# Kernel optimization log

Hardware: AMD Instinct MI355X
Metric: run time of the kernel (lower is better)

## Reference

```python
import jax, jax.numpy as jnp
import numpy as np
import math

QUERY_DIM = 128
SCALE = 1.0 / math.sqrt(QUERY_DIM)

def setup_inputs() -> dict:
    key = jax.random.key(0)
    k1, k2, k3 = jax.random.split(key, 3)
    B, Q, K, D = 16, 2048, 2048, 128
    return {
        "query": jax.random.normal(k1, (B, Q, D), dtype=jnp.float32),
        "keys": jax.random.normal(k2, (B, K, D), dtype=jnp.float32),
        "values": jax.random.normal(k3, (B, K, D), dtype=jnp.float32),
    }

def reference(query, keys, values):
    # energy[b,q,k] = sum_d query[b,q,d] * keys[b,k,d], scaled then softmax over k
    energy = jnp.einsum("bqd,bkd->bqk", query, keys) * SCALE
    attn = jax.nn.softmax(energy, axis=2)
    # linear combination over values
    return jnp.einsum("bqk,bkv->bqv", attn, values)
```

## Files before the change

kernel.cpp:

```cpp
#include <hip/hip_runtime.h>
#include <hip/hip_bf16.h>


#define BATCH 16
#define QLEN 2048
#define KLEN 2048
#define DIM 128
#define BM 64
#define BN 64
#define NT (KLEN / BN)

#define SMEM_BYTES 34048

typedef __attribute__((ext_vector_type(8))) short bf16x8;
typedef __attribute__((ext_vector_type(4))) float f32x4;

__device__ __forceinline__ short f2bf(float x) {
    union { float f; unsigned u; } v; v.f = x;
    unsigned r = v.u + 0x7FFFu + ((v.u >> 16) & 1u);
    return (short)(r >> 16);
}
__device__ __forceinline__ unsigned pkbf(float a, float b) {
    union { float f; unsigned u; } x, y; x.f = a; y.f = b;
    unsigned ra = x.u + 0x7FFFu + ((x.u >> 16) & 1u);
    unsigned rb = y.u + 0x7FFFu + ((y.u >> 16) & 1u);
    return __builtin_amdgcn_perm(rb, ra, 0x07060302u);
}
__device__ __forceinline__ float fexp2(float x) {
#if __has_builtin(__builtin_amdgcn_exp2f)
    return __builtin_amdgcn_exp2f(x);
#else
    return exp2f(x);
#endif
}

#define TSTR 72
__global__ __launch_bounds__(256) void prepass_kernel(
    const float* __restrict__ kg, const float* __restrict__ vg,
    unsigned short* __restrict__ Kws, unsigned short* __restrict__ Vtws)
{
    __shared__ unsigned short T[DIM * TSTR];
    const int tid = threadIdx.x;
    const int kb  = blockIdx.x * BN;
    const int b   = blockIdx.y;
    const float* kt = kg + ((size_t)b * KLEN + kb) * DIM;
    const float* vt = vg + ((size_t)b * KLEN + kb) * DIM;

    unsigned short* koF = Kws + ((size_t)b * KLEN + kb) * DIM;
#pragma unroll
    for (int j = 0; j < 4; ++j) {
        int c = tid + 256 * j;
        int key   = c & 63;
        int chunk = c >> 6;
        float4 k0 = *(const float4*)(kt + key * DIM + chunk * 8);
        float4 k1 = *(const float4*)(kt + key * DIM + chunk * 8 + 4);
        uint4 w;
        w.x = pkbf(k0.x, k0.y); w.y = pkbf(k0.z, k0.w);
        w.z = pkbf(k1.x, k1.y); w.w = pkbf(k1.z, k1.w);
        int r    = (key & 3) | ((key & 8) >> 1) | ((key & 16) >> 1)
                 | ((key & 4) << 2) | (key & 32);
        int kw_  = r >> 5;
        int half = (r >> 4) & 1;
        int lm_  = r & 15;
        int dk   = chunk >> 2;
        int qd   = chunk & 3;
        int soff = (((kw_ * 4 + dk) * 2 + half) * 4 + qd) * 128 + lm_ * 8;
        *(uint4*)(koF + soff) = w;
    }

#pragma unroll
    for (int j = 0; j < 8; ++j) {
        int idx = tid + 256 * j;
        int key = idx >> 5;
        int d4  = (idx & 31) * 4;
        float4 vv = *(const float4*)(vt + key * DIM + d4);
        T[(d4 + 0) * TSTR + key] = (unsigned short)f2bf(vv.x);
        T[(d4 + 1) * TSTR + key] = (unsigned short)f2bf(vv.y);
        T[(d4 + 2) * TSTR + key] = (unsigned short)f2bf(vv.z);
        T[(d4 + 3) * TSTR + key] = (unsigned short)f2bf(vv.w);
    }
    __syncthreads();
    unsigned short* voF = Vtws + ((size_t)b * KLEN + kb) * DIM;
#pragma unroll
    for (int j = 0; j < 4; ++j) {
        int c = tid + 256 * j;
        int d = c >> 3;
        int g = c & 7;
        uint4 u = *(const uint4*)&T[d * TSTR + g * 8];
        int kw_  = g >> 2;
        int qd   = g & 3;
        int dt   = d >> 4;
        int lm_  = d & 15;
        int soff = ((kw_ * 8 + dt) * 4 + qd) * 128 + lm_ * 8;
        *(uint4*)(voF + soff) = u;
    }
}

__global__ __launch_bounds__(256, 2) void attn_flash_kernel(
    const float* __restrict__ qg,
    const unsigned short* __restrict__ Kws,
    const unsigned short* __restrict__ Vtws,
    float* __restrict__ outg)
{
    __shared__ __align__(16) char SMC[SMEM_BYTES];

    const int tid  = threadIdx.x;
    const int wave = tid >> 6;
    const int lane = tid & 63;
    const int lm   = lane & 15;
    const int quad = lane >> 4;
    const int rw   = wave >> 1;
    const int kw   = wave & 1;

    const int n  = blockIdx.y * gridDim.x + blockIdx.x;
    const int np = (n & 7) * 64 + (n >> 3);
    const int b     = np >> 5;
    const int qbase = (np & 31) * BM + rw * 32;

    const float QSCALE = 0.08838834764831845f * 1.4426950408889634f;

    bf16x8 qfA[4], qfB[4];
    {
        const float* qrowA = qg + (size_t)(b * QLEN + qbase + lm) * DIM;
        const float* qrowB = qrowA + 16 * DIM;
#pragma unroll
        for (int dk = 0; dk < 4; ++dk) {
            int d0 = dk * 32 + quad * 8;
            float4 a = *(const float4*)(qrowA + d0);
            float4 c = *(const float4*)(qrowA + d0 + 4);
            uint4 u;
            u.x = pkbf(a.x*QSCALE, a.y*QSCALE); u.y = pkbf(a.z*QSCALE, a.w*QSCALE);
            u.z = pkbf(c.x*QSCALE, c.y*QSCALE); u.w = pkbf(c.z*QSCALE, c.w*QSCALE);
            qfA[dk] = *(bf16x8*)&u;
            float4 e = *(const float4*)(qrowB + d0);
            float4 g = *(const float4*)(qrowB + d0 + 4);
            uint4 v;
            v.x = pkbf(e.x*QSCALE, e.y*QSCALE); v.y = pkbf(e.z*QSCALE, e.w*QSCALE);
            v.z = pkbf(g.x*QSCALE, g.y*QSCALE); v.w = pkbf(g.z*QSCALE, g.w*QSCALE);
            qfB[dk] = *(bf16x8*)&v;
        }
    }

    f32x4 OA[8], OB[8];
#pragma unroll
    for (int i = 0; i < 8; ++i) { OA[i] = 0.0f; OB[i] = 0.0f; }
    float lrA = 0.f, lrB = 0.f;

    const unsigned short* kfp = Kws + (size_t)b * KLEN * DIM
                              + kw * 4096 + lane * 8;
    const unsigned short* vfp = Vtws + (size_t)b * KLEN * DIM
                              + kw * 4096 + lane * 8;

    f32x4 SP0a, SP1a, SP0b, SP1b;
    bf16x8 vp[8];
    bf16x8 kp[8];

#pragma unroll
    for (int i = 0; i < 8; ++i) kp[i] = *(const bf16x8*)(kfp + i * 512);
#pragma unroll
    for (int i = 0; i < 8; ++i) vp[i] = *(const bf16x8*)(vfp + i * 512);
    {
        f32x4 S0a = 0.0f, S1a = 0.0f, S0b = 0.0f, S1b = 0.0f;
#pragma unroll
        for (int dk = 0; dk < 4; ++dk) {
            S0a = __builtin_amdgcn_mfma_f32_16x16x32_bf16(kp[2*dk],   qfA[dk], S0a, 0, 0, 0);
            S0b = __builtin_amdgcn_mfma_f32_16x16x32_bf16(kp[2*dk],   qfB[dk], S0b, 0, 0, 0);
            S1a = __builtin_amdgcn_mfma_f32_16x16x32_bf16(kp[2*dk+1], qfA[dk], S1a, 0, 0, 0);
            S1b = __builtin_amdgcn_mfma_f32_16x16x32_bf16(kp[2*dk+1], qfB[dk], S1b, 0, 0, 0);
        }
#pragma unroll
        for (int i = 0; i < 8; ++i)
            kp[i] = *(const bf16x8*)(kfp + 8192 + i * 512);
        SP0a = S0a; SP1a = S1a; SP0b = S0b; SP1b = S1b;
    }

    for (int t = 1; t < NT; ++t) {
        float a0 = fexp2(SP0a[0]), a1 = fexp2(SP0a[1]), a2 = fexp2(SP0a[2]), a3 = fexp2(SP0a[3]);
        float a4 = fexp2(SP1a[0]), a5 = fexp2(SP1a[1]), a6 = fexp2(SP1a[2]), a7 = fexp2(SP1a[3]);
        float b0 = fexp2(SP0b[0]), b1 = fexp2(SP0b[1]), b2 = fexp2(SP0b[2]), b3 = fexp2(SP0b[3]);
        float b4 = fexp2(SP1b[0]), b5 = fexp2(SP1b[1]), b6 = fexp2(SP1b[2]), b7 = fexp2(SP1b[3]);
        uint4 puA, puB;
        puA.x = pkbf(a0,a1); puA.y = pkbf(a2,a3); puA.z = pkbf(a4,a5); puA.w = pkbf(a6,a7);
        puB.x = pkbf(b0,b1); puB.y = pkbf(b2,b3); puB.z = pkbf(b4,b5); puB.w = pkbf(b6,b7);
        bf16x8 pfA = *(bf16x8*)&puA;
        bf16x8 pfB = *(bf16x8*)&puB;
        lrA += ((a0+a1)+(a2+a3)) + ((a4+a5)+(a6+a7));
        lrB += ((b0+b1)+(b2+b3)) + ((b4+b5)+(b6+b7));

        f32x4 S0a = 0.0f, S1a = 0.0f, S0b = 0.0f, S1b = 0.0f;
#pragma unroll
        for (int dk = 0; dk < 4; ++dk) {
            S0a = __builtin_amdgcn_mfma_f32_16x16x32_bf16(kp[2*dk],   qfA[dk], S0a, 0, 0, 0);
            S0b = __builtin_amdgcn_mfma_f32_16x16x32_bf16(kp[2*dk],   qfB[dk], S0b, 0, 0, 0);
            S1a = __builtin_amdgcn_mfma_f32_16x16x32_bf16(kp[2*dk+1], qfA[dk], S1a, 0, 0, 0);
            S1b = __builtin_amdgcn_mfma_f32_16x16x32_bf16(kp[2*dk+1], qfB[dk], S1b, 0, 0, 0);
        }

        if (t + 1 < NT) {
            const unsigned short* kt1 = kfp + (size_t)(t + 1) * 8192;
#pragma unroll
            for (int i = 0; i < 8; ++i)
                kp[i] = *(const bf16x8*)(kt1 + i * 512);
        }

#pragma unroll
        for (int dt = 0; dt < 8; ++dt) {
            OA[dt] = __builtin_amdgcn_mfma_f32_16x16x32_bf16(vp[dt], pfA, OA[dt], 0, 0, 0);
            OB[dt] = __builtin_amdgcn_mfma_f32_16x16x32_bf16(vp[dt], pfB, OB[dt], 0, 0, 0);
        }

        {
            const unsigned short* vt1 = vfp + (size_t)t * 8192;
#pragma unroll
            for (int dt = 0; dt < 8; ++dt)
                vp[dt] = *(const bf16x8*)(vt1 + dt * 512);
        }

        SP0a = S0a; SP1a = S1a; SP0b = S0b; SP1b = S1b;
    }

    {
        float a0 = fexp2(SP0a[0]), a1 = fexp2(SP0a[1]), a2 = fexp2(SP0a[2]), a3 = fexp2(SP0a[3]);
        float a4 = fexp2(SP1a[0]), a5 = fexp2(SP1a[1]), a6 = fexp2(SP1a[2]), a7 = fexp2(SP1a[3]);
        float b0 = fexp2(SP0b[0]), b1 = fexp2(SP0b[1]), b2 = fexp2(SP0b[2]), b3 = fexp2(SP0b[3]);
        float b4 = fexp2(SP1b[0]), b5 = fexp2(SP1b[1]), b6 = fexp2(SP1b[2]), b7 = fexp2(SP1b[3]);
        uint4 puA, puB;
        puA.x = pkbf(a0,a1); puA.y = pkbf(a2,a3); puA.z = pkbf(a4,a5); puA.w = pkbf(a6,a7);
        puB.x = pkbf(b0,b1); puB.y = pkbf(b2,b3); puB.z = pkbf(b4,b5); puB.w = pkbf(b6,b7);
        bf16x8 pfA = *(bf16x8*)&puA;
        bf16x8 pfB = *(bf16x8*)&puB;
        lrA += ((a0+a1)+(a2+a3)) + ((a4+a5)+(a6+a7));
        lrB += ((b0+b1)+(b2+b3)) + ((b4+b5)+(b6+b7));
#pragma unroll
        for (int dt = 0; dt < 8; ++dt) {
            OA[dt] = __builtin_amdgcn_mfma_f32_16x16x32_bf16(vp[dt], pfA, OA[dt], 0, 0, 0);
            OB[dt] = __builtin_amdgcn_mfma_f32_16x16x32_bf16(vp[dt], pfB, OB[dt], 0, 0, 0);
        }
    }

    lrA += __shfl_xor(lrA, 16, 64); lrA += __shfl_xor(lrA, 32, 64);
    lrB += __shfl_xor(lrB, 16, 64); lrB += __shfl_xor(lrB, 32, 64);

    float* Orw = (float*)SMC + rw * 4288;
    if (kw == 1) {
#pragma unroll
        for (int dt = 0; dt < 8; ++dt) {
            *(f32x4*)&Orw[lm*132        + dt*16 + quad*4] = OA[dt];
            *(f32x4*)&Orw[(16+lm)*132   + dt*16 + quad*4] = OB[dt];
        }
        if (lane < 16)      Orw[4224 + lm]      = lrA;
        else if (lane < 32) Orw[4224 + 16 + lm] = lrB;
    }
    __syncthreads();
    if (kw == 0) {
        float invA = 1.0f / (lrA + Orw[4224 + lm]);
        float invB = 1.0f / (lrB + Orw[4224 + 16 + lm]);
        float* orowA = outg + (size_t)(b * QLEN + qbase + lm) * DIM;
        float* orowB = orowA + 16 * DIM;
#pragma unroll
        for (int dt = 0; dt < 8; ++dt) {
            f32x4 oA = *(const f32x4*)&Orw[lm*132      + dt*16 + quad*4];
            f32x4 oB = *(const f32x4*)&Orw[(16+lm)*132 + dt*16 + quad*4];
            *(f32x4*)&orowA[dt*16 + quad*4] = (OA[dt] + oA) * invA;
            *(f32x4*)&orowB[dt*16 + quad*4] = (OB[dt] + oB) * invB;
        }
    }
}

extern "C" void kernel_launch(void* const* d_in, const int* in_sizes, int n_in,
                              void* d_out, int out_size, void* d_ws, size_t ws_size,
                              hipStream_t stream) {
    const float* q = (const float*)d_in[0];
    const float* k = (const float*)d_in[1];
    const float* v = (const float*)d_in[2];
    float* o = (float*)d_out;
    unsigned short* Kws  = (unsigned short*)d_ws;
    unsigned short* Vtws = Kws + (size_t)BATCH * KLEN * DIM;
    dim3 grid(KLEN / BN, BATCH);
    prepass_kernel<<<grid, 256, 0, stream>>>(k, v, Kws, Vtws);
    dim3 grid2(QLEN / BM, BATCH);
    attn_flash_kernel<<<grid2, 256, 0, stream>>>(q, Kws, Vtws, o);
}
```

Before: 136.5 us.

## Split keys across four waves per row group with 512-thread blocks

```diff
diff --git a/kernel.cpp b/kernel.cpp
--- a/kernel.cpp
+++ b/kernel.cpp
@@ -7,10 +7,11 @@
 #define KLEN 2048
 #define DIM 128
 #define BM 64
-#define BN 64
-#define NT (KLEN / BN)
-
-#define SMEM_BYTES 34048
+#define BNW 128
+#define NT (KLEN / BNW)
+#define TILE_SHORTS 8192
+
+#define SMEM_BYTES 34304
 
 typedef __attribute__((ext_vector_type(8))) short bf16x8;
 typedef __attribute__((ext_vector_type(4))) float f32x4;
@@ -37,11 +38,11 @@
 #define TSTR 72
 __global__ __launch_bounds__(256) void prepass_kernel(
     const float* __restrict__ kg, const float* __restrict__ vg,
-    unsigned short* __restrict__ Kws, unsigned short* __restrict__ Vtws)
+    unsigned short* __restrict__ Kws, unsigned short* __restrict__ Vws)
 {
     __shared__ unsigned short T[DIM * TSTR];
     const int tid = threadIdx.x;
-    const int kb  = blockIdx.x * BN;
+    const int kb  = blockIdx.x * 64;
     const int b   = blockIdx.y;
     const float* kt = kg + ((size_t)b * KLEN + kb) * DIM;
     const float* vt = vg + ((size_t)b * KLEN + kb) * DIM;
@@ -59,12 +60,12 @@
         w.z = pkbf(k1.x, k1.y); w.w = pkbf(k1.z, k1.w);
         int r    = (key & 3) | ((key & 8) >> 1) | ((key & 16) >> 1)
                  | ((key & 4) << 2) | (key & 32);
-        int kw_  = r >> 5;
+        int kh   = r >> 5;
         int half = (r >> 4) & 1;
         int lm_  = r & 15;
         int dk   = chunk >> 2;
         int qd   = chunk & 3;
-        int soff = (((kw_ * 4 + dk) * 2 + half) * 4 + qd) * 128 + lm_ * 8;
+        int soff = (((kh * 4 + dk) * 2 + half) * 4 + qd) * 128 + lm_ * 8;
         *(uint4*)(koF + soff) = w;
     }
 
@@ -80,26 +81,26 @@
         T[(d4 + 3) * TSTR + key] = (unsigned short)f2bf(vv.w);
     }
     __syncthreads();
-    unsigned short* voF = Vtws + ((size_t)b * KLEN + kb) * DIM;
+    unsigned short* voF = Vws + ((size_t)b * KLEN + kb) * DIM;
 #pragma unroll
     for (int j = 0; j < 4; ++j) {
         int c = tid + 256 * j;
         int d = c >> 3;
         int g = c & 7;
         uint4 u = *(const uint4*)&T[d * TSTR + g * 8];
-        int kw_  = g >> 2;
+        int kh   = g >> 2;
         int qd   = g & 3;
         int dt   = d >> 4;
         int lm_  = d & 15;
-        int soff = ((kw_ * 8 + dt) * 4 + qd) * 128 + lm_ * 8;
+        int soff = ((kh * 8 + dt) * 4 + qd) * 128 + lm_ * 8;
         *(uint4*)(voF + soff) = u;
     }
 }
 
-__global__ __launch_bounds__(256, 2) void attn_flash_kernel(
+__global__ __launch_bounds__(512, 4) void attn_flash_kernel(
     const float* __restrict__ qg,
     const unsigned short* __restrict__ Kws,
-    const unsigned short* __restrict__ Vtws,
+    const unsigned short* __restrict__ Vws,
     float* __restrict__ outg)
 {
     __shared__ __align__(16) char SMC[SMEM_BYTES];
@@ -109,8 +110,8 @@
     const int lane = tid & 63;
     const int lm   = lane & 15;
     const int quad = lane >> 4;
-    const int rw   = wave >> 1;
-    const int kw   = wave & 1;
+    const int rw   = wave >> 2;
+    const int kw   = wave & 3;
 
     const int n  = blockIdx.y * gridDim.x + blockIdx.x;
     const int np = (n & 7) * 64 + (n >> 3);
@@ -146,10 +147,9 @@
     for (int i = 0; i < 8; ++i) { OA[i] = 0.0f; OB[i] = 0.0f; }
     float lrA = 0.f, lrB = 0.f;
 
-    const unsigned short* kfp = Kws + (size_t)b * KLEN * DIM
-                              + kw * 4096 + lane * 8;
-    const unsigned short* vfp = Vtws + (size_t)b * KLEN * DIM
-                              + kw * 4096 + lane * 8;
+    const size_t woff = (size_t)(kw >> 1) * TILE_SHORTS + (kw & 1) * 4096 + lane * 8;
+    const unsigned short* kfp = Kws + (size_t)b * KLEN * DIM + woff;
+    const unsigned short* vfp = Vws + (size_t)b * KLEN * DIM + woff;
 
     f32x4 SP0a, SP1a, SP0b, SP1b;
     bf16x8 vp[8];
@@ -170,7 +170,7 @@
         }
 #pragma unroll
         for (int i = 0; i < 8; ++i)
-            kp[i] = *(const bf16x8*)(kfp + 8192 + i * 512);
+            kp[i] = *(const bf16x8*)(kfp + 2 * TILE_SHORTS + i * 512);
         SP0a = S0a; SP1a = S1a; SP0b = S0b; SP1b = S1b;
     }
 
@@ -197,7 +197,7 @@
         }
 
         if (t + 1 < NT) {
-            const unsigned short* kt1 = kfp + (size_t)(t + 1) * 8192;
+            const unsigned short* kt1 = kfp + (size_t)(t + 1) * (2 * TILE_SHORTS);
 #pragma unroll
             for (int i = 0; i < 8; ++i)
                 kp[i] = *(const bf16x8*)(kt1 + i * 512);
@@ -210,7 +210,7 @@
         }
 
         {
-            const unsigned short* vt1 = vfp + (size_t)t * 8192;
+            const unsigned short* vt1 = vfp + (size_t)t * (2 * TILE_SHORTS);
 #pragma unroll
             for (int dt = 0; dt < 8; ++dt)
                 vp[dt] = *(const bf16x8*)(vt1 + dt * 512);
@@ -242,27 +242,38 @@
     lrB += __shfl_xor(lrB, 16, 64); lrB += __shfl_xor(lrB, 32, 64);
 
     float* Orw = (float*)SMC + rw * 4288;
-    if (kw == 1) {
-#pragma unroll
-        for (int dt = 0; dt < 8; ++dt) {
-            *(f32x4*)&Orw[lm*132        + dt*16 + quad*4] = OA[dt];
-            *(f32x4*)&Orw[(16+lm)*132   + dt*16 + quad*4] = OB[dt];
-        }
-        if (lane < 16)      Orw[4224 + lm]      = lrA;
-        else if (lane < 32) Orw[4224 + 16 + lm] = lrB;
-    }
-    __syncthreads();
+#pragma unroll
+    for (int s = 3; s >= 1; --s) {
+        if (kw == s) {
+#pragma unroll
+            for (int dt = 0; dt < 8; ++dt) {
+                *(f32x4*)&Orw[lm*132        + dt*16 + quad*4] = OA[dt];
+                *(f32x4*)&Orw[(16+lm)*132   + dt*16 + quad*4] = OB[dt];
+            }
+            if (lane < 16)      Orw[4224 + lm]      = lrA;
+            else if (lane < 32) Orw[4224 + 16 + lm] = lrB;
+        }
+        __syncthreads();
+        if (kw == s - 1) {
+#pragma unroll
+            for (int dt = 0; dt < 8; ++dt) {
+                OA[dt] += *(const f32x4*)&Orw[lm*132        + dt*16 + quad*4];
+                OB[dt] += *(const f32x4*)&Orw[(16+lm)*132   + dt*16 + quad*4];
+            }
+            lrA += Orw[4224 + lm];
+            lrB += Orw[4224 + 16 + lm];
+        }
+    }
+
     if (kw == 0) {
-        float invA = 1.0f / (lrA + Orw[4224 + lm]);
-        float invB = 1.0f / (lrB + Orw[4224 + 16 + lm]);
+        float invA = 1.0f / lrA;
+        float invB = 1.0f / lrB;
         float* orowA = outg + (size_t)(b * QLEN + qbase + lm) * DIM;
         float* orowB = orowA + 16 * DIM;
 #pragma unroll
         for (int dt = 0; dt < 8; ++dt) {
-            f32x4 oA = *(const f32x4*)&Orw[lm*132      + dt*16 + quad*4];
-            f32x4 oB = *(const f32x4*)&Orw[(16+lm)*132 + dt*16 + quad*4];
-            *(f32x4*)&orowA[dt*16 + quad*4] = (OA[dt] + oA) * invA;
-            *(f32x4*)&orowB[dt*16 + quad*4] = (OB[dt] + oB) * invB;
+            *(f32x4*)&orowA[dt*16 + quad*4] = OA[dt] * invA;
+            *(f32x4*)&orowB[dt*16 + quad*4] = OB[dt] * invB;
         }
     }
 }
@@ -274,10 +285,10 @@
     const float* k = (const float*)d_in[1];
     const float* v = (const float*)d_in[2];
     float* o = (float*)d_out;
-    unsigned short* Kws  = (unsigned short*)d_ws;
-    unsigned short* Vtws = Kws + (size_t)BATCH * KLEN * DIM;
-    dim3 grid(KLEN / BN, BATCH);
-    prepass_kernel<<<grid, 256, 0, stream>>>(k, v, Kws, Vtws);
+    unsigned short* Kws = (unsigned short*)d_ws;
+    unsigned short* Vws = Kws + (size_t)BATCH * KLEN * DIM;
+    dim3 grid(KLEN / 64, BATCH);
+    prepass_kernel<<<grid, 256, 0, stream>>>(k, v, Kws, Vws);
     dim3 grid2(QLEN / BM, BATCH);
-    attn_flash_kernel<<<grid2, 256, 0, stream>>>(q, Kws, Vtws, o);
-}
+    attn_flash_kernel<<<grid2, 512, 0, stream>>>(q, Kws, Vws, o);
+}
```

New measurement: 379.5 us. 178% more time.
